# Kernel optimization log

Hardware: AMD Instinct MI355X
Metric: run time of the kernel (lower is better)

Reference implementation:

```python
import jax, jax.numpy as jnp
import numpy as np
from jax import lax

D_MODEL = 96; D_STATE = 16; D_INNER = 192; DT_RANK = 6; K = 4
BSZ = 2; HH = 64; WW = 64


def setup_inputs() -> dict:
    key = jax.random.key(0)
    ks = jax.random.split(key, 16)
    f = lambda k, shape, s=0.02: (jax.random.normal(k, shape) * s).astype(jnp.float32)
    P = DT_RANK + 2 * D_STATE
    return {
        "x": jax.random.normal(ks[0], (BSZ, HH, WW, D_MODEL), jnp.float32),
        "W_in": f(ks[1], (2 * D_INNER, D_MODEL)),
        "b_in": jnp.zeros((2 * D_INNER,), jnp.float32),
        "conv_w": f(ks[2], (D_INNER, 1, 3, 3)),
        "conv_b": jnp.zeros((D_INNER,), jnp.float32),
        "W_xp": f(ks[3], (K * P, K * D_INNER)),
        "b_xp": jnp.zeros((K * P,), jnp.float32),
        "W_dt": f(ks[4], (K * D_INNER, K * DT_RANK)),
        "b_dt": f(ks[5], (K * D_INNER,), 0.1),
        "A_log": jax.random.normal(ks[6], (K * D_INNER, D_STATE), jnp.float32),
        "D_skip": jnp.ones((K * D_INNER,), jnp.float32),
        "dt_bias": jax.random.normal(ks[7], (K * D_INNER,), jnp.float32),
        "W_out": f(ks[8], (D_MODEL, D_INNER)),
        "b_out": jnp.zeros((D_MODEL,), jnp.float32),
        "gamma": jnp.ones((D_INNER,), jnp.float32),
        "beta": jnp.zeros((D_INNER,), jnp.float32),
    }


def cross_scan(x):
    # x: (B, D, H, W) -> (B, 4, D, L); dirs: row-major, col-major, and their reverses
    B, D, H, W = x.shape
    L = H * W
    x0 = x.reshape(B, D, L)
    x1 = jnp.swapaxes(x, 2, 3).reshape(B, D, L)
    return jnp.stack([x0, x1, x0[..., ::-1], x1[..., ::-1]], axis=1)


def cross_merge(ys):
    # ys: (B, 4, D, H, W) -> (B, D, L); inverse of cross_scan, summed
    B, Kk, D, H, W = ys.shape
    L = H * W
    yf = ys.reshape(B, Kk, D, L)
    y02 = yf[:, 0] + yf[:, 2, :, ::-1]
    y13 = yf[:, 1] + yf[:, 3, :, ::-1]
    y13 = jnp.swapaxes(y13.reshape(B, D, W, H), 2, 3).reshape(B, D, L)
    return y02 + y13


def selective_scan(u, dt, A, Bm, Cm, D_skip, dt_bias):
    # u, dt: (B,K,Dv,L); A: (K,Dv,N); Bm, Cm: (B,K,N,L); D_skip, dt_bias: (K,Dv)
    # NOTE: torch code repeats Bm/Cm across Dv; we broadcast instead (same math).
    dt = jax.nn.softplus(dt + dt_bias[None, :, :, None])
    dt_l = jnp.moveaxis(dt, -1, 0)   # (L,B,K,Dv)
    u_l = jnp.moveaxis(u, -1, 0)     # (L,B,K,Dv)
    B_l = jnp.moveaxis(Bm, -1, 0)    # (L,B,K,N)
    C_l = jnp.moveaxis(Cm, -1, 0)    # (L,B,K,N)

    def step(h, inp):
        dt_t, u_t, b_t, c_t = inp
        dA = jnp.exp(dt_t[..., None] * A[None])                 # (B,K,Dv,N)
        dBu = (dt_t * u_t)[..., None] * b_t[:, :, None, :]      # (B,K,Dv,N)
        h = dA * h + dBu
        y = jnp.einsum('bkdn,bkn->bkd', h, c_t)
        return h, y

    h0 = jnp.zeros(u.shape[:3] + (A.shape[-1],), u.dtype)
    _, ys = lax.scan(step, h0, (dt_l, u_l, B_l, C_l))
    ys = jnp.moveaxis(ys, 0, -1)  # (B,K,Dv,L)
    return ys + u * D_skip[None, :, :, None]


def reference(x, W_in, b_in, conv_w, conv_b, W_xp, b_xp, W_dt, b_dt,
              A_log, D_skip, dt_bias, W_out, b_out, gamma, beta):
    B, H, W, _ = x.shape
    L = H * W
    xz = x @ W_in.T + b_in
    xx, z = jnp.split(xz, 2, axis=-1)
    z = jax.nn.silu(z)
    xc = jnp.transpose(xx, (0, 3, 1, 2))  # (B, D, H, W)
    xc = lax.conv_general_dilated(xc, conv_w, (1, 1), 'SAME',
                                  feature_group_count=D_INNER,
                                  dimension_numbers=('NCHW', 'OIHW', 'NCHW'))
    xc = jax.nn.silu(xc + conv_b[None, :, None, None])

    xs = cross_scan(xc)                      # (B, K, D, L)
    xs_flat = xs.reshape(B, K * D_INNER, L)

    x_dbl = jnp.einsum('bcl,pc->bpl', xs_flat, W_xp) + b_xp[None, :, None]
    x_dbl = x_dbl.reshape(B, K, DT_RANK + 2 * D_STATE, L)
    dts, Bm, Cm = jnp.split(x_dbl, [DT_RANK, DT_RANK + D_STATE], axis=2)
    dts = dts.reshape(B, K * DT_RANK, L)
    dts = jnp.einsum('brl,dr->bdl', dts, W_dt) + b_dt[None, :, None]

    A = -jnp.exp(A_log).reshape(K, D_INNER, D_STATE)
    u = xs_flat.reshape(B, K, D_INNER, L)
    dt = dts.reshape(B, K, D_INNER, L)
    ys = selective_scan(u, dt, A, Bm, Cm,
                        D_skip.reshape(K, D_INNER), dt_bias.reshape(K, D_INNER))

    y = cross_merge(ys.reshape(B, K, D_INNER, H, W))  # (B, D, L)
    y = jnp.transpose(y.reshape(B, D_INNER, H, W), (0, 2, 3, 1))

    mu = jnp.mean(y, axis=-1, keepdims=True)
    var = jnp.mean(jnp.square(y - mu), axis=-1, keepdims=True)
    y = (y - mu) * lax.rsqrt(var + 1e-5) * gamma + beta
    y = y * z
    return y @ W_out.T + b_out
```

## Files before the change

kernel.cpp:

```cpp
#include <hip/hip_runtime.h>
#include <cstdint>
#include <cstddef>


#define CHUNK 32
#define NCK   128

#if __has_builtin(__builtin_amdgcn_exp2f)
#define EXP2(x) __builtin_amdgcn_exp2f(x)
#else
#define EXP2(x) exp2f(x)
#endif
#define LOG2E 1.44269504088896340736f
#define LN2   0.69314718055994530942f

typedef __attribute__((ext_vector_type(8))) short short8;
typedef __attribute__((ext_vector_type(8))) unsigned short ushort8;
typedef __attribute__((ext_vector_type(4))) float f32x4;

__device__ __forceinline__ float siluf(float x){ return x * (1.f/(1.f+__expf(-x))); }
__device__ __forceinline__ float softplus_fast(float v){
  float e  = EXP2(v*LOG2E);
  float sp = LN2*__log2f(1.f + e);
  return (v > 20.f) ? v : sp;
}
__device__ __forceinline__ unsigned short f2b(float f){
  uint32_t u = __float_as_uint(f);
  uint32_t r = (u + 0x7fffu + ((u>>16)&1u)) >> 16;
  return (unsigned short)r;
}
__device__ __forceinline__ short8 cast8(const float* p){
  float4 f0 = *(const float4*)p;
  float4 f1 = *(const float4*)(p+4);
  unsigned short t[8] = {f2b(f0.x),f2b(f0.y),f2b(f0.z),f2b(f0.w),
                         f2b(f1.x),f2b(f1.y),f2b(f1.z),f2b(f1.w)};
  return *(short8*)t;
}

__global__ __launch_bounds__(256) void k_pack(
    const float* __restrict__ Wxp, const float* __restrict__ Win,
    const float* __restrict__ Wout,
    unsigned short* __restrict__ Wf, unsigned short* __restrict__ Wfin,
    unsigned short* __restrict__ Wfout)
{
  int tid = blockIdx.x*256 + threadIdx.x;
  int lane = tid & 63;
  int n = lane & 15, q = lane >> 4;
  if (tid < 18432){
    int rest = tid >> 6;
    int pt = rest % 6; rest /= 6;
    int k32 = rest & 3; rest >>= 2;
    int kc = rest % 6; int ph = rest / 6;
    int p = ph*96 + pt*16 + n;
    int kbase = kc*128 + k32*32 + q*8;
    unsigned short v[8];
#pragma unroll
    for (int j = 0; j < 8; j++)
      v[j] = (p < 152) ? f2b(Wxp[(size_t)p*768 + kbase + j]) : (unsigned short)0;
    *(ushort8*)(Wf + (size_t)tid*8) = *(ushort8*)v;
  } else if (tid < 23040){
    int e = tid - 18432;
    int rest = e >> 6;
    int nt = rest % 24, k32 = rest / 24;
    int p = nt*16 + n;
    int kbase = k32*32 + q*8;
    unsigned short v[8];
#pragma unroll
    for (int j = 0; j < 8; j++) v[j] = f2b(Win[(size_t)p*96 + kbase + j]);
    *(ushort8*)(Wfin + (size_t)e*8) = *(ushort8*)v;
  } else if (tid < 25344){
    int e = tid - 23040;
    int rest = e >> 6;
    int nt = rest % 6, k32 = rest / 6;
    int p = nt*16 + n;
    int kbase = k32*32 + q*8;
    unsigned short v[8];
#pragma unroll
    for (int j = 0; j < 8; j++) v[j] = f2b(Wout[(size_t)p*192 + kbase + j]);
    *(ushort8*)(Wfout + (size_t)e*8) = *(ushort8*)v;
  }
}

__global__ __launch_bounds__(256) void k_gemm_in(
    const float* __restrict__ x, const unsigned short* __restrict__ Wfin,
    const float* __restrict__ bias, float* __restrict__ xx, float* __restrict__ zs)
{
  const int tid = threadIdx.x;
  const int lane = tid & 63, w = tid >> 6;
  const int m0 = blockIdx.x*64;
  const int n = lane & 15, q = lane >> 4;
  f32x4 acc[4][6] = {};
#pragma unroll
  for (int k32 = 0; k32 < 3; k32++){
    int kb = k32*32 + q*8;
    short8 a[4];
#pragma unroll
    for (int mf = 0; mf < 4; mf++)
      a[mf] = cast8(x + (size_t)(m0 + mf*16 + n)*96 + kb);
#pragma unroll
    for (int j = 0; j < 6; j++){
      int nt = w*6 + j;
      short8 bfr = *(const short8*)(Wfin + ((size_t)(k32*24 + nt)*64 + lane)*8);
#pragma unroll
      for (int mf = 0; mf < 4; mf++)
        acc[mf][j] = __builtin_amdgcn_mfma_f32_16x16x32_bf16(a[mf], bfr, acc[mf][j], 0, 0, 0);
    }
  }
#pragma unroll
  for (int mf = 0; mf < 4; mf++)
#pragma unroll
    for (int j = 0; j < 6; j++){
      int nn = w*96 + j*16 + n;
      float bv = bias[nn];
#pragma unroll
      for (int reg = 0; reg < 4; reg++){
        int l = m0 + mf*16 + q*4 + reg;
        float v = acc[mf][j][reg] + bv;
        if (nn < 192) xx[(size_t)l*192 + nn] = v;
        else          zs[(size_t)l*192 + (nn-192)] = siluf(v);
      }
    }
}

__global__ __launch_bounds__(256) void k_conv(
    const float* __restrict__ xx, const float* __restrict__ cw, const float* __restrict__ cb,
    float* __restrict__ xc,
    unsigned short* __restrict__ xcb, unsigned short* __restrict__ xcTb)
{
  int gid = blockIdx.x*256 + threadIdx.x;
  int c = gid % 192;
  int l = (gid/192) & 4095;
  int b = gid / (192*4096);
  int h = l >> 6, w = l & 63;
  float s = 0.f;
#pragma unroll
  for (int kh = 0; kh < 3; kh++){
    int h2 = h + kh - 1;
    if ((unsigned)h2 >= 64u) continue;
#pragma unroll
    for (int kw = 0; kw < 3; kw++){
      int w2 = w + kw - 1;
      if ((unsigned)w2 >= 64u) continue;
      s += xx[((size_t)b*4096 + h2*64 + w2)*192 + c] * cw[c*9 + kh*3 + kw];
    }
  }
  s = siluf(s + cb[c]);
  unsigned short sb = f2b(s);
  size_t i0 = ((size_t)b*4096 + l)*192 + c;
  xc[i0] = s; xcb[i0] = sb;
  int tl = (l & 63)*64 + (l >> 6);
  xcTb[((size_t)b*4096 + tl)*192 + c] = sb;
}

__global__ __launch_bounds__(256) void k_gemm_xdbl(
    const unsigned short* __restrict__ xcb, const unsigned short* __restrict__ xcTb,
    const unsigned short* __restrict__ Wf, const float* __restrict__ bxp,
    float* __restrict__ xdbl, float* __restrict__ dts_c)
{
  __shared__ unsigned short Bsh[4*6*64*8];
  const int tid = threadIdx.x;
  const int lane = tid & 63, w = tid >> 6;
  const int wl = w & 1, wp = w >> 1;
  const int l0 = blockIdx.x*64, ph = blockIdx.y, b = blockIdx.z;
  const int n = lane & 15, q = lane >> 4;
  f32x4 acc[2][3] = {};
  const unsigned short* slab0 = Wf + (size_t)ph*6*12288;
  for (int kc = 0; kc < 6; kc++){
    __syncthreads();
    const ushort8* srcp = (const ushort8*)(slab0 + (size_t)kc*12288);
#pragma unroll
    for (int t = 0; t < 6; t++) ((ushort8*)Bsh)[tid + t*256] = srcp[tid + t*256];
    __syncthreads();
#pragma unroll
    for (int k32 = 0; k32 < 4; k32++){
      int kk = kc*128 + k32*32;
      int dir = kk/192; int ch = kk%192 + q*8;
      const unsigned short* sp = (dir & 1) ? xcTb : xcb;
      bool rev = (dir >= 2);
      short8 a[2];
#pragma unroll
      for (int mt = 0; mt < 2; mt++){
        int ls = l0 + wl*32 + mt*16 + n;
        int row = rev ? 4095 - ls : ls;
        a[mt] = *(const short8*)(sp + ((size_t)b*4096 + row)*192 + ch);
      }
#pragma unroll
      for (int j = 0; j < 3; j++){
        short8 bfr = *(const short8*)&Bsh[((size_t)(k32*6 + wp*3 + j)*64 + lane)*8];
#pragma unroll
        for (int mt = 0; mt < 2; mt++)
          acc[mt][j] = __builtin_amdgcn_mfma_f32_16x16x32_bf16(a[mt], bfr, acc[mt][j], 0, 0, 0);
      }
    }
  }
#pragma unroll
  for (int mt = 0; mt < 2; mt++)
#pragma unroll
    for (int j = 0; j < 3; j++){
      int p = ph*96 + (wp*3+j)*16 + n;
      if (p < 152){
        int k = p/38, pp = p%38;
        int off = (pp < 6) ? pp : pp + 2;
        float bias = bxp[p];
#pragma unroll
        for (int reg = 0; reg < 4; reg++){
          int l = l0 + wl*32 + mt*16 + q*4 + reg;
          float val = acc[mt][j][reg] + bias;
          xdbl[(((size_t)b*4 + k)*4096 + l)*48 + off] = val;
          if (pp < 6) dts_c[((size_t)b*4096 + l)*24 + k*6 + pp] = val;
        }
      }
    }
}

__global__ __launch_bounds__(256) void k_scanA(
    const float* __restrict__ xc, const float* __restrict__ xdbl,
    const float* __restrict__ dts_c,
    const float* __restrict__ A_log, const float* __restrict__ Wdt,
    const float* __restrict__ bdt, const float* __restrict__ dtbias,
    float* __restrict__ dte, float* __restrict__ sdtb, float* __restrict__ Sb)
{
  const int lane = threadIdx.x & 63;
  const int wid  = __builtin_amdgcn_readfirstlane(blockIdx.x*4 + (threadIdx.x >> 6));
  const int ck = wid & (NCK-1); const int g = wid / NCK;
  const int dblk = g % 3; const int bk = g / 3;
  const int k = bk & 3; const int b = bk >> 2;
  const int d = dblk*64 + lane; const int ch = k*192 + d;
  float An[16];
  {
    const float4* ap = (const float4*)(A_log + (size_t)ch*16);
#pragma unroll
    for (int i = 0; i < 4; i++){
      float4 t = ap[i];
      An[4*i+0] = -LOG2E*__expf(t.x); An[4*i+1] = -LOG2E*__expf(t.y);
      An[4*i+2] = -LOG2E*__expf(t.z); An[4*i+3] = -LOG2E*__expf(t.w);
    }
  }
  float Wr[24];
#pragma unroll
  for (int r = 0; r < 24; r++) Wr[r] = Wdt[(size_t)ch*24 + r];
  const float bsum = bdt[ch] + dtbias[ch];
  const int l0 = ck*CHUNK;
  const bool rev = (k >= 2);
  const int tr = k & 1;
  const int T0 = tr ? ((l0 & 63)*64 + (l0 >> 6)) : l0;
  const int rs = tr ? 64 : 1;
  const int row0 = rev ? 4095 - T0 : T0;
  const int rstep = (rev ? -rs : rs)*192;
  const float* up  = xc + ((size_t)b*4096 + row0)*192 + d;
  const float* qc  = dts_c + ((size_t)b*4096 + l0)*24;
  const float* xbc = xdbl + (((size_t)b*4 + k)*4096 + l0)*48;
  float* dtw = dte + (((size_t)b*4 + k)*4096 + l0)*192 + d;
  float h[16];
#pragma unroll
  for (int n = 0; n < 16; n++) h[n] = 0.f;
  float sdt = 0.f;
#pragma unroll 4
  for (int t = 0; t < CHUNK; t++){
    float u  = up[0];
    float4 B0 = *(const float4*)(xbc + 8);
    float4 B1 = *(const float4*)(xbc + 12);
    float4 B2 = *(const float4*)(xbc + 16);
    float4 B3 = *(const float4*)(xbc + 20);
    float Bv[16] = {B0.x,B0.y,B0.z,B0.w, B1.x,B1.y,B1.z,B1.w,
                    B2.x,B2.y,B2.z,B2.w, B3.x,B3.y,B3.z,B3.w};
    float4 q0 = *(const float4*)(qc);
    float4 q1 = *(const float4*)(qc + 4);
    float4 q2 = *(const float4*)(qc + 8);
    float4 q3 = *(const float4*)(qc + 12);
    float4 q4 = *(const float4*)(qc + 16);
    float4 q5 = *(const float4*)(qc + 20);
    float qv[24] = {q0.x,q0.y,q0.z,q0.w, q1.x,q1.y,q1.z,q1.w,
                    q2.x,q2.y,q2.z,q2.w, q3.x,q3.y,q3.z,q3.w,
                    q4.x,q4.y,q4.z,q4.w, q5.x,q5.y,q5.z,q5.w};
    float v0 = bsum, v1 = 0.f, v2 = 0.f, v3 = 0.f;
#pragma unroll
    for (int r = 0; r < 24; r += 4){
      v0 = fmaf(Wr[r+0], qv[r+0], v0);
      v1 = fmaf(Wr[r+1], qv[r+1], v1);
      v2 = fmaf(Wr[r+2], qv[r+2], v2);
      v3 = fmaf(Wr[r+3], qv[r+3], v3);
    }
    float dt = softplus_fast((v0+v1) + (v2+v3));
    dtw[0] = dt;
    float dtu = dt*u;
    sdt += dt;
#pragma unroll
    for (int n = 0; n < 16; n++){
      float dA = EXP2(dt*An[n]);
      h[n] = fmaf(dA, h[n], dtu*Bv[n]);
    }
    qc += 24; xbc += 48; up += rstep; dtw += 192;
  }
  size_t base = ((size_t)wid*16)*64 + lane;
  sdtb[(size_t)wid*64 + lane] = sdt;
#pragma unroll
  for (int n = 0; n < 16; n++) Sb[base + n*64] = h[n];
}

__global__ __launch_bounds__(64) void k_scanB(
    const float* __restrict__ A_log, const float* __restrict__ sdtb,
    const float* __restrict__ Sb, float* __restrict__ H0)
{
  int tid = blockIdx.x*64 + threadIdx.x;
  int lane = tid & 63; int n = (tid >> 6) & 15; int g = tid >> 10;
  int dblk = g % 3; int bk = g / 3; int k = bk & 3;
  int ch = k*192 + dblk*64 + lane;
  float An = -LOG2E*__expf(A_log[(size_t)ch*16 + n]);
  float h = 0.f;
#pragma unroll 8
  for (int ck = 0; ck < NCK; ck++){
    size_t sidx = ((size_t)(g*NCK + ck))*64 + lane;
    size_t idx  = (((size_t)(g*NCK + ck)*16) + n)*64 + lane;
    H0[idx] = h;
    h = fmaf(EXP2(An*sdtb[sidx]), h, Sb[idx]);
  }
}

__global__ __launch_bounds__(256) void k_scanC(
    const float* __restrict__ xc, const float* __restrict__ xdbl,
    const float* __restrict__ A_log, const float* __restrict__ dte,
    const float* __restrict__ Dskip,
    const float* __restrict__ H0, float* __restrict__ ys)
{
  const int lane = threadIdx.x & 63;
  const int wid  = __builtin_amdgcn_readfirstlane(blockIdx.x*4 + (threadIdx.x >> 6));
  const int ck = wid & (NCK-1); const int g = wid / NCK;
  const int dblk = g % 3; const int bk = g / 3;
  const int k = bk & 3; const int b = bk >> 2;
  const int d = dblk*64 + lane; const int ch = k*192 + d;
  float An[16];
  {
    const float4* ap = (const float4*)(A_log + (size_t)ch*16);
#pragma unroll
    for (int i = 0; i < 4; i++){
      float4 t = ap[i];
      An[4*i+0] = -LOG2E*__expf(t.x); An[4*i+1] = -LOG2E*__expf(t.y);
      An[4*i+2] = -LOG2E*__expf(t.z); An[4*i+3] = -LOG2E*__expf(t.w);
    }
  }
  const float Dv = Dskip[ch];
  const int l0 = ck*CHUNK;
  const bool rev = (k >= 2);
  const int tr = k & 1;
  const int T0 = tr ? ((l0 & 63)*64 + (l0 >> 6)) : l0;
  const int rs = tr ? 64 : 1;
  const int row0 = rev ? 4095 - T0 : T0;
  const int rstep = (rev ? -rs : rs)*192;
  const float* up  = xc + ((size_t)b*4096 + row0)*192 + d;
  const float* xbc = xdbl + (((size_t)b*4 + k)*4096 + l0)*48;
  const float* dtp = dte + (((size_t)b*4 + k)*4096 + l0)*192 + d;
  float* ysp = ys + ((size_t)(k*2 + b))*4096*192 + (size_t)row0*192 + d;
  float h[16];
  size_t base = ((size_t)wid*16)*64 + lane;
#pragma unroll
  for (int n = 0; n < 16; n++) h[n] = H0[base + n*64];
#pragma unroll 4
  for (int t = 0; t < CHUNK; t++){
    float u  = up[0];
    float dt = dtp[0];
    float4 B0 = *(const float4*)(xbc + 8);
    float4 B1 = *(const float4*)(xbc + 12);
    float4 B2 = *(const float4*)(xbc + 16);
    float4 B3 = *(const float4*)(xbc + 20);
    float4 C0 = *(const float4*)(xbc + 24);
    float4 C1 = *(const float4*)(xbc + 28);
    float4 C2 = *(const float4*)(xbc + 32);
    float4 C3 = *(const float4*)(xbc + 36);
    float Bv[16] = {B0.x,B0.y,B0.z,B0.w, B1.x,B1.y,B1.z,B1.w,
                    B2.x,B2.y,B2.z,B2.w, B3.x,B3.y,B3.z,B3.w};
    float Cv[16] = {C0.x,C0.y,C0.z,C0.w, C1.x,C1.y,C1.z,C1.w,
                    C2.x,C2.y,C2.z,C2.w, C3.x,C3.y,C3.z,C3.w};
    float dtu = dt*u;
    float y0 = u*Dv, y1 = 0.f;
#pragma unroll
    for (int n = 0; n < 16; n += 2){
      float dA0 = EXP2(dt*An[n]);
      float dA1 = EXP2(dt*An[n+1]);
      h[n]   = fmaf(dA0, h[n],   dtu*Bv[n]);
      h[n+1] = fmaf(dA1, h[n+1], dtu*Bv[n+1]);
      y0 = fmaf(h[n],   Cv[n],   y0);
      y1 = fmaf(h[n+1], Cv[n+1], y1);
    }
    ysp[0] = y0 + y1;
    xbc += 48; dtp += 192; up += rstep; ysp += rstep;
  }
}

__global__ __launch_bounds__(256) void k_ln(
    const float* __restrict__ ys, const float* __restrict__ zs,
    const float* __restrict__ gamma, const float* __restrict__ beta,
    float* __restrict__ yln)
{
  int row = blockIdx.x*4 + (threadIdx.x >> 6);
  int lane = threadIdx.x & 63;
  int b = row >> 12; int l = row & 4095;
  float v[3];
#pragma unroll
  for (int j = 0; j < 3; j++){
    int c = lane + j*64;
    float s = 0.f;
#pragma unroll
    for (int k = 0; k < 4; k++) s += ys[(((size_t)k*2 + b)*4096 + l)*192 + c];
    v[j] = s;
  }
  float tot = v[0] + v[1] + v[2];
#pragma unroll
  for (int o = 1; o < 64; o <<= 1) tot += __shfl_xor(tot, o);
  float mean = tot * (1.f/192.f);
  float d0 = v[0]-mean, d1 = v[1]-mean, d2 = v[2]-mean;
  float vs = d0*d0 + d1*d1 + d2*d2;
#pragma unroll
  for (int o = 1; o < 64; o <<= 1) vs += __shfl_xor(vs, o);
  float rstd = rsqrtf(vs*(1.f/192.f) + 1e-5f);
  float nd[3] = {d0, d1, d2};
#pragma unroll
  for (int j = 0; j < 3; j++){
    int c = lane + j*64;
    float val = nd[j]*rstd*gamma[c] + beta[c];
    val *= zs[(size_t)row*192 + c];
    yln[(size_t)row*192 + c] = val;
  }
}

__global__ __launch_bounds__(256) void k_gemm_out(
    const float* __restrict__ yln, const unsigned short* __restrict__ Wfout,
    const float* __restrict__ bout, float* __restrict__ out)
{
  const int tid = threadIdx.x;
  const int lane = tid & 63, w = tid >> 6;
  const int m0 = blockIdx.x*64 + w*16;
  const int n = lane & 15, q = lane >> 4;
  f32x4 acc[6] = {};
#pragma unroll
  for (int k32 = 0; k32 < 6; k32++){
    int kb = k32*32 + q*8;
    short8 a = cast8(yln + (size_t)(m0 + n)*192 + kb);
#pragma unroll
    for (int j = 0; j < 6; j++){
      short8 bfr = *(const short8*)(Wfout + ((size_t)(k32*6 + j)*64 + lane)*8);
      acc[j] = __builtin_amdgcn_mfma_f32_16x16x32_bf16(a, bfr, acc[j], 0, 0, 0);
    }
  }
#pragma unroll
  for (int j = 0; j < 6; j++){
    int nn = j*16 + n;
    float bv = bout[nn];
#pragma unroll
    for (int reg = 0; reg < 4; reg++){
      int m = m0 + q*4 + reg;
      out[(size_t)m*96 + nn] = acc[j][reg] + bv;
    }
  }
}

extern "C" void kernel_launch(void* const* d_in, const int* in_sizes, int n_in,
                              void* d_out, int out_size, void* d_ws, size_t ws_size,
                              hipStream_t stream)
{
  const float* x      = (const float*)d_in[0];
  const float* W_in   = (const float*)d_in[1];
  const float* b_in   = (const float*)d_in[2];
  const float* conv_w = (const float*)d_in[3];
  const float* conv_b = (const float*)d_in[4];
  const float* W_xp   = (const float*)d_in[5];
  const float* b_xp   = (const float*)d_in[6];
  const float* W_dt   = (const float*)d_in[7];
  const float* b_dt   = (const float*)d_in[8];
  const float* A_log  = (const float*)d_in[9];
  const float* D_skip = (const float*)d_in[10];
  const float* dt_bias= (const float*)d_in[11];
  const float* W_out  = (const float*)d_in[12];
  const float* b_out  = (const float*)d_in[13];
  const float* gamma  = (const float*)d_in[14];
  const float* beta   = (const float*)d_in[15];
  float* out = (float*)d_out;

  float* ws    = (float*)d_ws;
  float* xx    = ws;
  float* zs    = ws + 1572864;
  float* xc    = ws + 3145728;
  float* xdbl  = ws + 4718592;
  float* ysb   = ws + 6291456;
  float* yln   = ws + 12582912;
  float* dte   = ws + 14155776;
  float* Sb    = ws + 20447232;
  float* H0    = ws + 23592960;
  float* sdtb  = ws + 26738688;
  float* dts_c = ws + 26935296;
  unsigned short* xcb   = (unsigned short*)(ws + 27131904);
  unsigned short* xcTb  = xcb + 1572864;
  unsigned short* Wf    = (unsigned short*)(ws + 28704768);
  unsigned short* Wfin  = (unsigned short*)(ws + 28778496);
  unsigned short* Wfout = (unsigned short*)(ws + 28796928);

  k_pack     <<<99,             256, 0, stream>>>(W_xp, W_in, W_out, Wf, Wfin, Wfout);
  k_gemm_in  <<<128,            256, 0, stream>>>(x, Wfin, b_in, xx, zs);
  k_conv     <<<6144,           256, 0, stream>>>(xx, conv_w, conv_b, xc, xcb, xcTb);
  k_gemm_xdbl<<<dim3(64, 2, 2), 256, 0, stream>>>(xcb, xcTb, Wf, b_xp, xdbl, dts_c);
  k_scanA    <<<768,            256, 0, stream>>>(xc, xdbl, dts_c, A_log, W_dt, b_dt, dt_bias, dte, sdtb, Sb);
  k_scanB    <<<384,            64,  0, stream>>>(A_log, sdtb, Sb, H0);
  k_scanC    <<<768,            256, 0, stream>>>(xc, xdbl, A_log, dte, D_skip, H0, ysb);
  k_ln       <<<2048,           256, 0, stream>>>(ysb, zs, gamma, beta, yln);
  k_gemm_out <<<128,            256, 0, stream>>>(yln, Wfout, b_out, out);
}
```

Before: 210.0 us.

## Compute local scan outputs in pass A and correct with carried state in pass C

The first chunked-scan pass now also computes each chunk's zero-initial-state output (including the D skip term) and stores it, together with the running cumulative dt, in an interleaved buffer. The final pass no longer redoes the recurrence. It adds the contribution of the carried-in state as C·exp(A·cumsum dt)·h0 on top of the stored local output. This removes the second recurrence and the reloads of u and B, at the cost of writing and reading a buffer twice the size of the old dt buffer and doing more work in pass A.

```diff
diff --git a/kernel.cpp b/kernel.cpp
--- a/kernel.cpp
+++ b/kernel.cpp
@@ -218,7 +218,8 @@
     const float* __restrict__ dts_c,
     const float* __restrict__ A_log, const float* __restrict__ Wdt,
     const float* __restrict__ bdt, const float* __restrict__ dtbias,
-    float* __restrict__ dte, float* __restrict__ sdtb, float* __restrict__ Sb)
+    const float* __restrict__ Dskip,
+    float* __restrict__ ylcs, float* __restrict__ sdtb, float* __restrict__ Sb)
 {
   const int lane = threadIdx.x & 63;
   const int wid  = __builtin_amdgcn_readfirstlane(blockIdx.x*4 + (threadIdx.x >> 6));
@@ -240,6 +241,7 @@
 #pragma unroll
   for (int r = 0; r < 24; r++) Wr[r] = Wdt[(size_t)ch*24 + r];
   const float bsum = bdt[ch] + dtbias[ch];
+  const float Dv = Dskip[ch];
   const int l0 = ck*CHUNK;
   const bool rev = (k >= 2);
   const int tr = k & 1;
@@ -250,7 +252,7 @@
   const float* up  = xc + ((size_t)b*4096 + row0)*192 + d;
   const float* qc  = dts_c + ((size_t)b*4096 + l0)*24;
   const float* xbc = xdbl + (((size_t)b*4 + k)*4096 + l0)*48;
-  float* dtw = dte + (((size_t)b*4 + k)*4096 + l0)*192 + d;
+  float* ylp = ylcs + ((((size_t)b*4 + k)*4096 + l0)*192 + d)*2;
   float h[16];
 #pragma unroll
   for (int n = 0; n < 16; n++) h[n] = 0.f;
@@ -262,8 +264,14 @@
     float4 B1 = *(const float4*)(xbc + 12);
     float4 B2 = *(const float4*)(xbc + 16);
     float4 B3 = *(const float4*)(xbc + 20);
+    float4 C0 = *(const float4*)(xbc + 24);
+    float4 C1 = *(const float4*)(xbc + 28);
+    float4 C2 = *(const float4*)(xbc + 32);
+    float4 C3 = *(const float4*)(xbc + 36);
     float Bv[16] = {B0.x,B0.y,B0.z,B0.w, B1.x,B1.y,B1.z,B1.w,
                     B2.x,B2.y,B2.z,B2.w, B3.x,B3.y,B3.z,B3.w};
+    float Cv[16] = {C0.x,C0.y,C0.z,C0.w, C1.x,C1.y,C1.z,C1.w,
+                    C2.x,C2.y,C2.z,C2.w, C3.x,C3.y,C3.z,C3.w};
     float4 q0 = *(const float4*)(qc);
     float4 q1 = *(const float4*)(qc + 4);
     float4 q2 = *(const float4*)(qc + 8);
@@ -282,15 +290,22 @@
       v3 = fmaf(Wr[r+3], qv[r+3], v3);
     }
     float dt = softplus_fast((v0+v1) + (v2+v3));
-    dtw[0] = dt;
     float dtu = dt*u;
     sdt += dt;
-#pragma unroll
-    for (int n = 0; n < 16; n++){
-      float dA = EXP2(dt*An[n]);
-      h[n] = fmaf(dA, h[n], dtu*Bv[n]);
-    }
-    qc += 24; xbc += 48; up += rstep; dtw += 192;
+    float y0 = dtu ? 0.f : 0.f;
+    y0 = u*Dv;
+    float y1 = 0.f;
+#pragma unroll
+    for (int n = 0; n < 16; n += 2){
+      float dA0 = EXP2(dt*An[n]);
+      float dA1 = EXP2(dt*An[n+1]);
+      h[n]   = fmaf(dA0, h[n],   dtu*Bv[n]);
+      h[n+1] = fmaf(dA1, h[n+1], dtu*Bv[n+1]);
+      y0 = fmaf(h[n],   Cv[n],   y0);
+      y1 = fmaf(h[n+1], Cv[n+1], y1);
+    }
+    *(float2*)ylp = make_float2(y0 + y1, sdt);
+    qc += 24; xbc += 48; up += rstep; ylp += 384;
   }
   size_t base = ((size_t)wid*16)*64 + lane;
   sdtb[(size_t)wid*64 + lane] = sdt;
@@ -318,10 +333,9 @@
 }
 
 __global__ __launch_bounds__(256) void k_scanC(
-    const float* __restrict__ xc, const float* __restrict__ xdbl,
-    const float* __restrict__ A_log, const float* __restrict__ dte,
-    const float* __restrict__ Dskip,
-    const float* __restrict__ H0, float* __restrict__ ys)
+    const float* __restrict__ xdbl, const float* __restrict__ A_log,
+    const float* __restrict__ ylcs, const float* __restrict__ H0,
+    float* __restrict__ ys)
 {
   const int lane = threadIdx.x & 63;
   const int wid  = __builtin_amdgcn_readfirstlane(blockIdx.x*4 + (threadIdx.x >> 6));
@@ -339,7 +353,6 @@
       An[4*i+2] = -LOG2E*__expf(t.z); An[4*i+3] = -LOG2E*__expf(t.w);
     }
   }
-  const float Dv = Dskip[ch];
   const int l0 = ck*CHUNK;
   const bool rev = (k >= 2);
   const int tr = k & 1;
@@ -347,43 +360,33 @@
   const int rs = tr ? 64 : 1;
   const int row0 = rev ? 4095 - T0 : T0;
   const int rstep = (rev ? -rs : rs)*192;
-  const float* up  = xc + ((size_t)b*4096 + row0)*192 + d;
   const float* xbc = xdbl + (((size_t)b*4 + k)*4096 + l0)*48;
-  const float* dtp = dte + (((size_t)b*4 + k)*4096 + l0)*192 + d;
+  const float* ylp = ylcs + ((((size_t)b*4 + k)*4096 + l0)*192 + d)*2;
   float* ysp = ys + ((size_t)(k*2 + b))*4096*192 + (size_t)row0*192 + d;
-  float h[16];
+  float h0r[16];
   size_t base = ((size_t)wid*16)*64 + lane;
 #pragma unroll
-  for (int n = 0; n < 16; n++) h[n] = H0[base + n*64];
+  for (int n = 0; n < 16; n++) h0r[n] = H0[base + n*64];
 #pragma unroll 4
   for (int t = 0; t < CHUNK; t++){
-    float u  = up[0];
-    float dt = dtp[0];
-    float4 B0 = *(const float4*)(xbc + 8);
-    float4 B1 = *(const float4*)(xbc + 12);
-    float4 B2 = *(const float4*)(xbc + 16);
-    float4 B3 = *(const float4*)(xbc + 20);
+    float2 yc = *(const float2*)ylp;
     float4 C0 = *(const float4*)(xbc + 24);
     float4 C1 = *(const float4*)(xbc + 28);
     float4 C2 = *(const float4*)(xbc + 32);
     float4 C3 = *(const float4*)(xbc + 36);
-    float Bv[16] = {B0.x,B0.y,B0.z,B0.w, B1.x,B1.y,B1.z,B1.w,
-                    B2.x,B2.y,B2.z,B2.w, B3.x,B3.y,B3.z,B3.w};
     float Cv[16] = {C0.x,C0.y,C0.z,C0.w, C1.x,C1.y,C1.z,C1.w,
                     C2.x,C2.y,C2.z,C2.w, C3.x,C3.y,C3.z,C3.w};
-    float dtu = dt*u;
-    float y0 = u*Dv, y1 = 0.f;
+    float cs = yc.y;
+    float y0 = yc.x, y1 = 0.f;
 #pragma unroll
     for (int n = 0; n < 16; n += 2){
-      float dA0 = EXP2(dt*An[n]);
-      float dA1 = EXP2(dt*An[n+1]);
-      h[n]   = fmaf(dA0, h[n],   dtu*Bv[n]);
-      h[n+1] = fmaf(dA1, h[n+1], dtu*Bv[n+1]);
-      y0 = fmaf(h[n],   Cv[n],   y0);
-      y1 = fmaf(h[n+1], Cv[n+1], y1);
+      float e0 = EXP2(An[n]*cs)   * h0r[n];
+      float e1 = EXP2(An[n+1]*cs) * h0r[n+1];
+      y0 = fmaf(Cv[n],   e0, y0);
+      y1 = fmaf(Cv[n+1], e1, y1);
     }
     ysp[0] = y0 + y1;
-    xbc += 48; dtp += 192; up += rstep; ysp += rstep;
+    ylp += 384; xbc += 48; ysp += rstep;
   }
 }
 
@@ -483,24 +486,24 @@
   float* xdbl  = ws + 4718592;
   float* ysb   = ws + 6291456;
   float* yln   = ws + 12582912;
-  float* dte   = ws + 14155776;
-  float* Sb    = ws + 20447232;
-  float* H0    = ws + 23592960;
-  float* sdtb  = ws + 26738688;
-  float* dts_c = ws + 26935296;
-  unsigned short* xcb   = (unsigned short*)(ws + 27131904);
+  float* Sb    = ws + 14155776;
+  float* H0    = ws + 17301504;
+  float* sdtb  = ws + 20447232;
+  float* dts_c = ws + 20643840;
+  float* ylcs  = ws + 20840448;
+  unsigned short* xcb   = (unsigned short*)(ws + 33423360);
   unsigned short* xcTb  = xcb + 1572864;
-  unsigned short* Wf    = (unsigned short*)(ws + 28704768);
-  unsigned short* Wfin  = (unsigned short*)(ws + 28778496);
-  unsigned short* Wfout = (unsigned short*)(ws + 28796928);
+  unsigned short* Wf    = (unsigned short*)(ws + 34996224);
+  unsigned short* Wfin  = (unsigned short*)(ws + 35069952);
+  unsigned short* Wfout = (unsigned short*)(ws + 35088384);
 
   k_pack     <<<99,             256, 0, stream>>>(W_xp, W_in, W_out, Wf, Wfin, Wfout);
   k_gemm_in  <<<128,            256, 0, stream>>>(x, Wfin, b_in, xx, zs);
   k_conv     <<<6144,           256, 0, stream>>>(xx, conv_w, conv_b, xc, xcb, xcTb);
   k_gemm_xdbl<<<dim3(64, 2, 2), 256, 0, stream>>>(xcb, xcTb, Wf, b_xp, xdbl, dts_c);
-  k_scanA    <<<768,            256, 0, stream>>>(xc, xdbl, dts_c, A_log, W_dt, b_dt, dt_bias, dte, sdtb, Sb);
+  k_scanA    <<<768,            256, 0, stream>>>(xc, xdbl, dts_c, A_log, W_dt, b_dt, dt_bias, D_skip, ylcs, sdtb, Sb);
   k_scanB    <<<384,            64,  0, stream>>>(A_log, sdtb, Sb, H0);
-  k_scanC    <<<768,            256, 0, stream>>>(xc, xdbl, A_log, dte, D_skip, H0, ysb);
+  k_scanC    <<<768,            256, 0, stream>>>(xdbl, A_log, ylcs, H0, ysb);
   k_ln       <<<2048,           256, 0, stream>>>(ysb, zs, gamma, beta, yln);
   k_gemm_out <<<128,            256, 0, stream>>>(yln, Wfout, b_out, out);
 }
```

Measured after the change: 209.5 us. Within noise of the previous version (-0.3%).
